# Performance work log

Measured on AMD Instinct MI355X. Metric: run time of the kernel, lower is better.

## Reference

```python
import jax, jax.numpy as jnp
import numpy as np

N = 100000
E = 800000
F_IN = 256
HID = 64
H = 4
NEG_SLOPE = 0.2
BN_EPS = 1e-5


def setup_inputs() -> dict:
    key = jax.random.key(0)
    ks = jax.random.split(key, 20)
    s = 0.05
    return {
        "x": jax.random.normal(ks[0], (N, F_IN), jnp.float32),
        "edge_index": jax.random.randint(ks[1], (2, E), 0, N, jnp.int64),
        # GCNConv params
        "W_gcn": jax.random.normal(ks[2], (F_IN, HID), jnp.float32) * s,
        "b_gcn": jnp.zeros((HID,), jnp.float32),
        "g0": jnp.ones((HID,), jnp.float32),
        "beta0": jnp.zeros((HID,), jnp.float32),
        # GATConv 1 params
        "W1": jax.random.normal(ks[3], (HID, H * HID), jnp.float32) * s,
        "a_src1": jax.random.normal(ks[4], (H, HID), jnp.float32) * s,
        "a_dst1": jax.random.normal(ks[5], (H, HID), jnp.float32) * s,
        "b1": jnp.zeros((H * HID,), jnp.float32),
        "g1": jnp.ones((H * HID,), jnp.float32),
        "beta1": jnp.zeros((H * HID,), jnp.float32),
        # GATConv 2 params
        "W2": jax.random.normal(ks[6], (H * HID, H * HID), jnp.float32) * s,
        "a_src2": jax.random.normal(ks[7], (H, HID), jnp.float32) * s,
        "a_dst2": jax.random.normal(ks[8], (H, HID), jnp.float32) * s,
        "b2": jnp.zeros((H * HID,), jnp.float32),
        "g2": jnp.ones((H * HID,), jnp.float32),
        "beta2": jnp.zeros((H * HID,), jnp.float32),
    }


def _add_self_loops(edge_index, n):
    loop = jnp.arange(n, dtype=edge_index.dtype)
    src = jnp.concatenate([edge_index[0], loop])
    dst = jnp.concatenate([edge_index[1], loop])
    return src, dst


def _batch_norm(x, g, b):
    # BatchNorm1d, training-mode batch stats (biased variance), no dropout
    m = x.mean(0)
    v = x.var(0)
    return g * (x - m) * jax.lax.rsqrt(v + BN_EPS) + b


def _gcn_conv(x, src, dst, W, b, n):
    # symmetric normalization with self-loops already included in src/dst
    deg = jax.ops.segment_sum(jnp.ones_like(dst, jnp.float32), dst, n)
    dinv = jax.lax.rsqrt(jnp.maximum(deg, 1.0))
    norm = dinv[src] * dinv[dst]  # [E']
    h = x @ W  # [N, HID]
    out = jax.ops.segment_sum(h[src] * norm[:, None], dst, n)
    return out + b


def _gat_conv(x, src, dst, W, a_src, a_dst, b, n):
    h = (x @ W).reshape(n, H, HID)  # [N, H, C]
    alpha_s = jnp.einsum("nhc,hc->nh", h, a_src)  # [N, H]
    alpha_d = jnp.einsum("nhc,hc->nh", h, a_dst)
    e = alpha_s[src] + alpha_d[dst]  # [E', H]
    e = jnp.where(e > 0, e, NEG_SLOPE * e)  # LeakyReLU
    # softmax over incoming edges of each dst node, per head
    emax = jax.ops.segment_max(e, dst, n)
    w = jnp.exp(e - emax[dst])
    wsum = jax.ops.segment_sum(w, dst, n)
    att = w / wsum[dst]  # [E', H]
    out = jax.ops.segment_sum(att[:, :, None] * h[src], dst, n)  # [N, H, C]
    return out.reshape(n, H * HID) + b


def reference(x, edge_index, W_gcn, b_gcn, g0, beta0, W1, a_src1, a_dst1, b1,
              g1, beta1, W2, a_src2, a_dst2, b2, g2, beta2):
    n = x.shape[0]
    src, dst = _add_self_loops(edge_index, n)
    h = jax.nn.relu(_gcn_conv(x, src, dst, W_gcn, b_gcn, n))
    h = _batch_norm(h, g0, beta0)
    h = _gat_conv(h, src, dst, W1, a_src1, a_dst1, b1, n)
    h = jax.nn.elu(_batch_norm(h, g1, beta1))
    h = _gat_conv(h, src, dst, W2, a_src2, a_dst2, b2, n)
    h = jax.nn.elu(_batch_norm(h, g2, beta2))
    return h
```

## Files before the change

kernel.cpp:

```cpp
#include <hip/hip_runtime.h>
#include <hip/hip_bf16.h>
#include <math.h>

#define NN 100000
#define EE 800000
#define FIN 256
#define CH 64
#define C1 256
#define BN_EPS 1e-5f
#define NEG_SLOPE 0.2f

typedef __attribute__((ext_vector_type(8))) short short8;
typedef __attribute__((ext_vector_type(8))) unsigned short u16x8;
typedef __attribute__((ext_vector_type(4))) float f32x4;

__device__ __forceinline__ float bf2f(ushort u) {
    return __uint_as_float(((unsigned)u) << 16);
}
__device__ __forceinline__ ushort f2bf(float f) {
    unsigned u = __float_as_uint(f);
    return (ushort)((u + 0x7FFF + ((u >> 16) & 1)) >> 16);
}

__global__ void hist_kernel(const int* __restrict__ ei, int* __restrict__ deg) {
    int t = blockIdx.x * 256 + threadIdx.x;
    if (t < EE) atomicAdd(&deg[ei[EE + t]], 1);
}
__global__ void dinv_kernel(const int* __restrict__ deg, float* __restrict__ dinv) {
    int i = blockIdx.x * 256 + threadIdx.x;
    if (i < NN) dinv[i] = rsqrtf((float)(deg[i] + 1));
}
__global__ void scan_k1(const int* __restrict__ deg, int* __restrict__ row_start,
                        int* __restrict__ bsum) {
    __shared__ int sh[256];
    int t = threadIdx.x;
    int i = blockIdx.x * 256 + t;
    int v = (i < NN) ? (deg[i] + 1) : 0;
    sh[t] = v;
    __syncthreads();
    for (int off = 1; off < 256; off <<= 1) {
        int add = (t >= off) ? sh[t - off] : 0;
        __syncthreads();
        sh[t] += add;
        __syncthreads();
    }
    if (i < NN) row_start[i] = sh[t] - v;
    if (t == 255) bsum[blockIdx.x] = sh[255];
}
__global__ void scan_k2(int* __restrict__ bsum, int nb) {
    __shared__ int sh[512];
    int t = threadIdx.x;
    int v = (t < nb) ? bsum[t] : 0;
    sh[t] = v;
    __syncthreads();
    for (int off = 1; off < 512; off <<= 1) {
        int add = (t >= off) ? sh[t - off] : 0;
        __syncthreads();
        sh[t] += add;
        __syncthreads();
    }
    if (t < nb) bsum[t] = sh[t] - v;
}
__global__ void scan_k3(int* __restrict__ row_start, const int* __restrict__ bsum) {
    int i = blockIdx.x * 256 + threadIdx.x;
    if (i < NN) row_start[i] += bsum[i >> 8];
    if (i == NN) row_start[NN] = EE + NN;
}
__global__ void scatter_kernel(const int* __restrict__ ei, const int* __restrict__ row_start,
                               int* __restrict__ fill, int* __restrict__ sorted) {
    int t = blockIdx.x * 256 + threadIdx.x;
    if (t >= EE + NN) return;
    int s, d;
    if (t < EE) { s = ei[t]; d = ei[EE + t]; }
    else        { s = t - EE; d = s; }
    int pos = atomicAdd(&fill[d], 1);
    sorted[row_start[d] + pos] = s;
}

__global__ void convert_f32_bf16(const float* __restrict__ in, ushort* __restrict__ out, long n4) {
    long i = (long)blockIdx.x * 256 + threadIdx.x;
    if (i < n4) {
        float4 v = *(const float4*)&in[i * 4];
        ushort4 o;
        o.x = f2bf(v.x); o.y = f2bf(v.y); o.z = f2bf(v.z); o.w = f2bf(v.w);
        *(ushort4*)&out[i * 4] = o;
    }
}
__global__ void transpose_w(const float* __restrict__ W, ushort* __restrict__ Bt, int M, int K) {
    int idx = blockIdx.x * 256 + threadIdx.x;
    if (idx < M * K) {
        int m = idx / K, n = idx % K;
        Bt[n * M + m] = f2bf(W[idx]);
    }
}

__global__ __launch_bounds__(256) void gemm_mfma(
        const ushort* __restrict__ A, const ushort* __restrict__ Bt,
        ushort* __restrict__ C, int M, int K) {
    __shared__ ushort As[64][40];
    __shared__ ushort Bs[64][40];
    int t = threadIdx.x;
    int w = t >> 6;
    int l = t & 63;
    int rowBase = blockIdx.y * 64;
    int colBase = blockIdx.x * 64;
    int srow = t >> 2;
    int sk = (t & 3) * 8;
    int m = l & 15, q = l >> 4;
    f32x4 acc[4] = {};
    for (int k0 = 0; k0 < M; k0 += 32) {
        uint4 av = make_uint4(0u, 0u, 0u, 0u);
        int gr = rowBase + srow;
        if (gr < NN) av = *(const uint4*)&A[(long)gr * M + k0 + sk];
        uint4 bv = *(const uint4*)&Bt[(long)(colBase + srow) * M + k0 + sk];
        *(uint4*)&As[srow][sk] = av;
        *(uint4*)&Bs[srow][sk] = bv;
        __syncthreads();
        short8 af = *(const short8*)&As[w * 16 + m][q * 8];
#pragma unroll
        for (int c = 0; c < 4; ++c) {
            short8 bf = *(const short8*)&Bs[c * 16 + m][q * 8];
            acc[c] = __builtin_amdgcn_mfma_f32_16x16x32_bf16(af, bf, acc[c], 0, 0, 0);
        }
        __syncthreads();
    }
#pragma unroll
    for (int c = 0; c < 4; ++c) {
#pragma unroll
        for (int r = 0; r < 4; ++r) {
            int orow = rowBase + w * 16 + q * 4 + r;
            if (orow < NN) C[(long)orow * K + colBase + c * 16 + m] = f2bf(acc[c][r]);
        }
    }
}

__global__ __launch_bounds__(256) void gcn_gather(
        const int* __restrict__ row_start, const int* __restrict__ sorted,
        const float* __restrict__ dinv, const ushort* __restrict__ h0,
        float* __restrict__ agg) {
    int node = blockIdx.x * 4 + (threadIdx.x >> 6);
    if (node >= NN) return;
    int l = threadIdx.x & 63;
    int slot = l >> 3;
    int li = l & 7;
    int c = li * 8;
    int b = row_start[node], e = row_start[node + 1];
    float a[8] = {};
    for (int i = b + slot; i < e; i += 8) {
        int s = sorted[i];
        float dv = dinv[s];
        u16x8 v = *(const u16x8*)&h0[(long)s * 64 + c];
#pragma unroll
        for (int j = 0; j < 8; ++j) a[j] += dv * bf2f((ushort)v[j]);
    }
#pragma unroll
    for (int j = 0; j < 8; ++j) {
        a[j] += __shfl_xor(a[j], 8);
        a[j] += __shfl_xor(a[j], 16);
        a[j] += __shfl_xor(a[j], 32);
    }
    if (slot == 0) {
        float dn = dinv[node];
        f32x4 o0, o1;
#pragma unroll
        for (int j = 0; j < 4; ++j) { o0[j] = a[j] * dn; o1[j] = a[4 + j] * dn; }
        *(f32x4*)&agg[(long)node * 64 + c] = o0;
        *(f32x4*)&agg[(long)node * 64 + c + 4] = o1;
    }
}

__global__ __launch_bounds__(256) void bn_stats64(
        const float* __restrict__ x, const float* __restrict__ bias,
        float* __restrict__ sums, float* __restrict__ sumsq) {
    __shared__ float red[4][16][8];
    int l = threadIdx.x & 63;
    int w = threadIdx.x >> 6;
    int wv = blockIdx.x * 4 + w;
    int nw = gridDim.x * 4;
    int sub = l >> 4;
    int c = (l & 15) * 4;
    f32x4 b4 = *(const f32x4*)&bias[c];
    float s0 = 0.f, s1 = 0.f, s2 = 0.f, s3 = 0.f;
    float q0 = 0.f, q1 = 0.f, q2 = 0.f, q3 = 0.f;
    for (int r = wv * 4 + sub; r < NN; r += nw * 4) {
        f32x4 v = *(const f32x4*)&x[(long)r * 64 + c];
        float v0 = fmaxf(v[0] + b4[0], 0.f);
        float v1 = fmaxf(v[1] + b4[1], 0.f);
        float v2 = fmaxf(v[2] + b4[2], 0.f);
        float v3 = fmaxf(v[3] + b4[3], 0.f);
        s0 += v0; s1 += v1; s2 += v2; s3 += v3;
        q0 += v0 * v0; q1 += v1 * v1; q2 += v2 * v2; q3 += v3 * v3;
    }
    s0 += __shfl_xor(s0, 16); s1 += __shfl_xor(s1, 16);
    s2 += __shfl_xor(s2, 16); s3 += __shfl_xor(s3, 16);
    q0 += __shfl_xor(q0, 16); q1 += __shfl_xor(q1, 16);
    q2 += __shfl_xor(q2, 16); q3 += __shfl_xor(q3, 16);
    s0 += __shfl_xor(s0, 32); s1 += __shfl_xor(s1, 32);
    s2 += __shfl_xor(s2, 32); s3 += __shfl_xor(s3, 32);
    q0 += __shfl_xor(q0, 32); q1 += __shfl_xor(q1, 32);
    q2 += __shfl_xor(q2, 32); q3 += __shfl_xor(q3, 32);
    if (sub == 0) {
        int li = l & 15;
        red[w][li][0] = s0; red[w][li][1] = s1; red[w][li][2] = s2; red[w][li][3] = s3;
        red[w][li][4] = q0; red[w][li][5] = q1; red[w][li][6] = q2; red[w][li][7] = q3;
    }
    __syncthreads();
    if (w == 0 && sub == 0) {
        int li = l & 15;
        atomicAdd(&sums[c + 0], red[0][li][0] + red[1][li][0] + red[2][li][0] + red[3][li][0]);
        atomicAdd(&sums[c + 1], red[0][li][1] + red[1][li][1] + red[2][li][1] + red[3][li][1]);
        atomicAdd(&sums[c + 2], red[0][li][2] + red[1][li][2] + red[2][li][2] + red[3][li][2]);
        atomicAdd(&sums[c + 3], red[0][li][3] + red[1][li][3] + red[2][li][3] + red[3][li][3]);
        atomicAdd(&sumsq[c + 0], red[0][li][4] + red[1][li][4] + red[2][li][4] + red[3][li][4]);
        atomicAdd(&sumsq[c + 1], red[0][li][5] + red[1][li][5] + red[2][li][5] + red[3][li][5]);
        atomicAdd(&sumsq[c + 2], red[0][li][6] + red[1][li][6] + red[2][li][6] + red[3][li][6]);
        atomicAdd(&sumsq[c + 3], red[0][li][7] + red[1][li][7] + red[2][li][7] + red[3][li][7]);
    }
}
__global__ __launch_bounds__(256) void bn_stats256(
        const ushort* __restrict__ x,
        float* __restrict__ sums, float* __restrict__ sumsq) {
    __shared__ float red[4][64][8];
    int l = threadIdx.x & 63;
    int w = threadIdx.x >> 6;
    int wv = blockIdx.x * 4 + w;
    int nw = gridDim.x * 4;
    int c = l * 4;
    float s0 = 0.f, s1 = 0.f, s2 = 0.f, s3 = 0.f;
    float q0 = 0.f, q1 = 0.f, q2 = 0.f, q3 = 0.f;
    for (int r = wv; r < NN; r += nw) {
        ushort4 v = *(const ushort4*)&x[(long)r * 256 + c];
        float v0 = bf2f(v.x), v1 = bf2f(v.y), v2 = bf2f(v.z), v3 = bf2f(v.w);
        s0 += v0; s1 += v1; s2 += v2; s3 += v3;
        q0 += v0 * v0; q1 += v1 * v1; q2 += v2 * v2; q3 += v3 * v3;
    }
    red[w][l][0] = s0; red[w][l][1] = s1; red[w][l][2] = s2; red[w][l][3] = s3;
    red[w][l][4] = q0; red[w][l][5] = q1; red[w][l][6] = q2; red[w][l][7] = q3;
    __syncthreads();
    if (w == 0) {
        atomicAdd(&sums[c + 0], red[0][l][0] + red[1][l][0] + red[2][l][0] + red[3][l][0]);
        atomicAdd(&sums[c + 1], red[0][l][1] + red[1][l][1] + red[2][l][1] + red[3][l][1]);
        atomicAdd(&sums[c + 2], red[0][l][2] + red[1][l][2] + red[2][l][2] + red[3][l][2]);
        atomicAdd(&sums[c + 3], red[0][l][3] + red[1][l][3] + red[2][l][3] + red[3][l][3]);
        atomicAdd(&sumsq[c + 0], red[0][l][4] + red[1][l][4] + red[2][l][4] + red[3][l][4]);
        atomicAdd(&sumsq[c + 1], red[0][l][5] + red[1][l][5] + red[2][l][5] + red[3][l][5]);
        atomicAdd(&sumsq[c + 2], red[0][l][6] + red[1][l][6] + red[2][l][6] + red[3][l][6]);
        atomicAdd(&sumsq[c + 3], red[0][l][7] + red[1][l][7] + red[2][l][7] + red[3][l][7]);
    }
}
__global__ void bn_finalize(const float* __restrict__ sums, const float* __restrict__ sumsq,
                            const float* __restrict__ g, const float* __restrict__ beta,
                            float* __restrict__ scale, float* __restrict__ shift, int C) {
    int c = threadIdx.x;
    if (c < C) {
        float mean = sums[c] / (float)NN;
        float var = sumsq[c] / (float)NN - mean * mean;
        float sc = g[c] * rsqrtf(var + BN_EPS);
        scale[c] = sc;
        shift[c] = beta[c] - mean * sc;
    }
}
__global__ __launch_bounds__(256) void bn_apply_gcn(
        const float* __restrict__ x, const float* __restrict__ bias,
        const float* __restrict__ scale, const float* __restrict__ shift,
        ushort* __restrict__ out) {
    int l = threadIdx.x & 63;
    int wv = blockIdx.x * 4 + (threadIdx.x >> 6);
    int nw = gridDim.x * 4;
    int c = (l & 15) * 4;
    int sub = l >> 4;
    f32x4 b4  = *(const f32x4*)&bias[c];
    f32x4 sc4 = *(const f32x4*)&scale[c];
    f32x4 sh4 = *(const f32x4*)&shift[c];
    for (int r = wv * 4 + sub; r < NN; r += nw * 4) {
        f32x4 v = *(const f32x4*)&x[(long)r * 64 + c];
        ushort4 o;
        o.x = f2bf(sc4[0] * fmaxf(v[0] + b4[0], 0.f) + sh4[0]);
        o.y = f2bf(sc4[1] * fmaxf(v[1] + b4[1], 0.f) + sh4[1]);
        o.z = f2bf(sc4[2] * fmaxf(v[2] + b4[2], 0.f) + sh4[2]);
        o.w = f2bf(sc4[3] * fmaxf(v[3] + b4[3], 0.f) + sh4[3]);
        *(ushort4*)&out[(long)r * 64 + c] = o;
    }
}
__global__ __launch_bounds__(256) void bn_apply_gat(
        const ushort* __restrict__ x,
        const float* __restrict__ scale, const float* __restrict__ shift,
        void* __restrict__ out, int out_bf16) {
    int l = threadIdx.x & 63;
    int wv = blockIdx.x * 4 + (threadIdx.x >> 6);
    int nw = gridDim.x * 4;
    int c = l * 4;
    f32x4 sc4 = *(const f32x4*)&scale[c];
    f32x4 sh4 = *(const f32x4*)&shift[c];
    if (out_bf16) {
        ushort* ob = (ushort*)out;
        for (int r = wv; r < NN; r += nw) {
            ushort4 v = *(const ushort4*)&x[(long)r * 256 + c];
            float t0 = sc4[0] * bf2f(v.x) + sh4[0];
            float t1 = sc4[1] * bf2f(v.y) + sh4[1];
            float t2 = sc4[2] * bf2f(v.z) + sh4[2];
            float t3 = sc4[3] * bf2f(v.w) + sh4[3];
            t0 = (t0 > 0.f) ? t0 : (__expf(t0) - 1.f);
            t1 = (t1 > 0.f) ? t1 : (__expf(t1) - 1.f);
            t2 = (t2 > 0.f) ? t2 : (__expf(t2) - 1.f);
            t3 = (t3 > 0.f) ? t3 : (__expf(t3) - 1.f);
            ushort4 o;
            o.x = f2bf(t0); o.y = f2bf(t1); o.z = f2bf(t2); o.w = f2bf(t3);
            *(ushort4*)&ob[(long)r * 256 + c] = o;
        }
    } else {
        float* of = (float*)out;
        for (int r = wv; r < NN; r += nw) {
            ushort4 v = *(const ushort4*)&x[(long)r * 256 + c];
            float t0 = sc4[0] * bf2f(v.x) + sh4[0];
            float t1 = sc4[1] * bf2f(v.y) + sh4[1];
            float t2 = sc4[2] * bf2f(v.z) + sh4[2];
            float t3 = sc4[3] * bf2f(v.w) + sh4[3];
            f32x4 o;
            o[0] = (t0 > 0.f) ? t0 : (__expf(t0) - 1.f);
            o[1] = (t1 > 0.f) ? t1 : (__expf(t1) - 1.f);
            o[2] = (t2 > 0.f) ? t2 : (__expf(t2) - 1.f);
            o[3] = (t3 > 0.f) ? t3 : (__expf(t3) - 1.f);
            *(f32x4*)&of[(long)r * 256 + c] = o;
        }
    }
}

__global__ void gat_alpha(const ushort* __restrict__ h, const float* __restrict__ a_src,
                          const float* __restrict__ a_dst,
                          float* __restrict__ alpha_s, float* __restrict__ alpha_d) {
    int n = blockIdx.x;
    int t = threadIdx.x;
    float hv = bf2f(h[(long)n * 256 + t]);
    float vs = hv * a_src[t];
    float vd = hv * a_dst[t];
    for (int off = 32; off > 0; off >>= 1) {
        vs += __shfl_down(vs, off);
        vd += __shfl_down(vd, off);
    }
    if ((t & 63) == 0) {
        int head = t >> 6;
        alpha_s[n * 4 + head] = vs;
        alpha_d[n * 4 + head] = vd;
    }
}

__global__ __launch_bounds__(256) void gat_att(
        const int* __restrict__ row_start, const int* __restrict__ sorted,
        const float* __restrict__ as, const float* __restrict__ ad,
        float* __restrict__ att, float* __restrict__ inv_ls) {
    int node = blockIdx.x * 4 + (threadIdx.x >> 6);
    if (node >= NN) return;
    int l = threadIdx.x & 63;
    int h = l & 3, k = l >> 2;
    int b = row_start[node], e = row_start[node + 1];
    float adn = ad[node * 4 + h];
    float lm = -1e30f;
    for (int i = b + k; i < e; i += 16) {
        int s = sorted[i];
        float ev = as[s * 4 + h] + adn;
        ev = (ev > 0.f) ? ev : NEG_SLOPE * ev;
        lm = fmaxf(lm, ev);
    }
    lm = fmaxf(lm, __shfl_xor(lm, 4));
    lm = fmaxf(lm, __shfl_xor(lm, 8));
    lm = fmaxf(lm, __shfl_xor(lm, 16));
    lm = fmaxf(lm, __shfl_xor(lm, 32));
    float ls = 0.f;
    for (int i = b + k; i < e; i += 16) {
        int s = sorted[i];
        float ev = as[s * 4 + h] + adn;
        ev = (ev > 0.f) ? ev : NEG_SLOPE * ev;
        float wv = __expf(ev - lm);
        att[(long)i * 4 + h] = wv;
        ls += wv;
    }
    ls += __shfl_xor(ls, 4);
    ls += __shfl_xor(ls, 8);
    ls += __shfl_xor(ls, 16);
    ls += __shfl_xor(ls, 32);
    if (k == 0) inv_ls[node * 4 + h] = 1.0f / ls;
}

__global__ __launch_bounds__(256) void gat_gather(
        const int* __restrict__ row_start, const int* __restrict__ sorted,
        const float* __restrict__ att, const float* __restrict__ inv_ls,
        const ushort* __restrict__ h, ushort* __restrict__ out) {
    int node = blockIdx.x * 4 + (threadIdx.x >> 6);
    if (node >= NN) return;
    int l = threadIdx.x & 63;
    int slot = l >> 5;
    int li = l & 31;
    int c = li * 8;
    int head = li >> 3;
    int b = row_start[node], e = row_start[node + 1];
    float a[8] = {};
    int i = b + slot;
    for (; i + 2 < e; i += 4) {
        int s0 = sorted[i], s1 = sorted[i + 2];
        float w0 = att[(long)i * 4 + head];
        float w1 = att[(long)(i + 2) * 4 + head];
        u16x8 v0 = *(const u16x8*)&h[(long)s0 * 256 + c];
        u16x8 v1 = *(const u16x8*)&h[(long)s1 * 256 + c];
#pragma unroll
        for (int j = 0; j < 8; ++j)
            a[j] += w0 * bf2f((ushort)v0[j]) + w1 * bf2f((ushort)v1[j]);
    }
    for (; i < e; i += 2) {
        int s0 = sorted[i];
        float w0 = att[(long)i * 4 + head];
        u16x8 v0 = *(const u16x8*)&h[(long)s0 * 256 + c];
#pragma unroll
        for (int j = 0; j < 8; ++j) a[j] += w0 * bf2f((ushort)v0[j]);
    }
#pragma unroll
    for (int j = 0; j < 8; ++j) a[j] += __shfl_xor(a[j], 32);
    if (slot == 0) {
        float inv = inv_ls[node * 4 + head];
        u16x8 o;
#pragma unroll
        for (int j = 0; j < 8; ++j) o[j] = f2bf(a[j] * inv);
        *(u16x8*)&out[(long)node * 256 + c] = o;
    }
}

extern "C" void kernel_launch(void* const* d_in, const int* in_sizes, int n_in,
                              void* d_out, int out_size, void* d_ws, size_t ws_size,
                              hipStream_t stream) {
    const float* x      = (const float*)d_in[0];
    const int*   ei     = (const int*)d_in[1];
    const float* W_gcn  = (const float*)d_in[2];
    const float* b_gcn  = (const float*)d_in[3];
    const float* g0     = (const float*)d_in[4];
    const float* beta0  = (const float*)d_in[5];
    const float* W1     = (const float*)d_in[6];
    const float* a_src1 = (const float*)d_in[7];
    const float* a_dst1 = (const float*)d_in[8];
    const float* b1     = (const float*)d_in[9];
    const float* g1     = (const float*)d_in[10];
    const float* beta1  = (const float*)d_in[11];
    const float* W2     = (const float*)d_in[12];
    const float* a_src2 = (const float*)d_in[13];
    const float* a_dst2 = (const float*)d_in[14];
    const float* b2     = (const float*)d_in[15];
    const float* g2     = (const float*)d_in[16];
    const float* beta2  = (const float*)d_in[17];

    const long N = NN;
    float* ws = (float*)d_ws;

    float* dinv    = ws;
    float* alpha_s = ws + N;
    float* alpha_d = ws + 5 * N;
    float* sums    = ws + 9 * N;
    float* sumsq   = sums + 256;
    float* scale   = sumsq + 256;
    float* shift   = scale + 256;
    int*   row_start = (int*)(shift + 256);
    int*   fill      = row_start + NN + 1;
    int*   deg_i     = fill + NN;
    int*   sorted    = deg_i + NN;
    int*   bsum      = sorted + EE + NN;
    ushort* Wgt  = (ushort*)(ws + 23 * N);
    ushort* W1t  = Wgt + 16384;
    ushort* W2t  = W1t + 16384;
    ushort* h0b  = (ushort*)(ws + 24 * N);
    ushort* x1b  = h0b;
    float*  agg0 = ws + 56 * N;
    ushort* h1b  = (ushort*)(ws + 120 * N);
    ushort* x2b  = (ushort*)(ws + 248 * N);
    ushort* xb   = x2b;
    ushort* yb   = (ushort*)(ws + 376 * N);
    float*  attb = ws + 504 * N;
    float*  inv_ls = ws + 540 * N;
    float*  outp = (float*)d_out;

    const int BLK = 256;
    dim3 blk(BLK);
    const int NBLK_N = (NN + 255) / 256;

    hipMemsetAsync(fill, 0, 2L * NN * sizeof(int), stream);
    hist_kernel<<<(EE + 255) / 256, blk, 0, stream>>>(ei, deg_i);
    dinv_kernel<<<NBLK_N, blk, 0, stream>>>(deg_i, dinv);
    scan_k1<<<NBLK_N, blk, 0, stream>>>(deg_i, row_start, bsum);
    scan_k2<<<1, 512, 0, stream>>>(bsum, NBLK_N);
    scan_k3<<<(NN + 1 + 255) / 256, blk, 0, stream>>>(row_start, bsum);
    scatter_kernel<<<(EE + NN + 255) / 256, blk, 0, stream>>>(ei, row_start, fill, sorted);

    convert_f32_bf16<<<(int)((N * 256 / 4 + 255) / 256), blk, 0, stream>>>(x, xb, N * 256 / 4);
    transpose_w<<<(FIN * CH + 255) / 256, blk, 0, stream>>>(W_gcn, Wgt, FIN, CH);
    transpose_w<<<(CH * C1 + 255) / 256, blk, 0, stream>>>(W1, W1t, CH, C1);
    transpose_w<<<(C1 * C1 + 255) / 256, blk, 0, stream>>>(W2, W2t, C1, C1);

    gemm_mfma<<<dim3(CH / 64, (NN + 63) / 64), blk, 0, stream>>>(xb, Wgt, h0b, FIN, CH);
    gcn_gather<<<(NN + 3) / 4, blk, 0, stream>>>(row_start, sorted, dinv, h0b, agg0);
    hipMemsetAsync(sums, 0, 512 * sizeof(float), stream);
    bn_stats64<<<512, blk, 0, stream>>>(agg0, b_gcn, sums, sumsq);
    bn_finalize<<<1, CH, 0, stream>>>(sums, sumsq, g0, beta0, scale, shift, CH);
    bn_apply_gcn<<<1024, blk, 0, stream>>>(agg0, b_gcn, scale, shift, x1b);

    gemm_mfma<<<dim3(C1 / 64, (NN + 63) / 64), blk, 0, stream>>>(x1b, W1t, h1b, CH, C1);
    gat_alpha<<<NN, blk, 0, stream>>>(h1b, a_src1, a_dst1, alpha_s, alpha_d);
    gat_att<<<(NN + 3) / 4, blk, 0, stream>>>(row_start, sorted, alpha_s, alpha_d, attb, inv_ls);
    gat_gather<<<(NN + 3) / 4, blk, 0, stream>>>(row_start, sorted, attb, inv_ls, h1b, yb);
    hipMemsetAsync(sums, 0, 512 * sizeof(float), stream);
    bn_stats256<<<512, blk, 0, stream>>>(yb, sums, sumsq);
    bn_finalize<<<1, C1, 0, stream>>>(sums, sumsq, g1, beta1, scale, shift, C1);
    bn_apply_gat<<<2048, blk, 0, stream>>>(yb, scale, shift, x2b, 1);

    gemm_mfma<<<dim3(C1 / 64, (NN + 63) / 64), blk, 0, stream>>>(x2b, W2t, h1b, C1, C1);
    gat_alpha<<<NN, blk, 0, stream>>>(h1b, a_src2, a_dst2, alpha_s, alpha_d);
    gat_att<<<(NN + 3) / 4, blk, 0, stream>>>(row_start, sorted, alpha_s, alpha_d, attb, inv_ls);
    gat_gather<<<(NN + 3) / 4, blk, 0, stream>>>(row_start, sorted, attb, inv_ls, h1b, yb);
    hipMemsetAsync(sums, 0, 512 * sizeof(float), stream);
    bn_stats256<<<512, blk, 0, stream>>>(yb, sums, sumsq);
    bn_finalize<<<1, C1, 0, stream>>>(sums, sumsq, g2, beta2, scale, shift, C1);
    bn_apply_gat<<<2048, blk, 0, stream>>>(yb, scale, shift, outp, 0);
}
```

Baseline: 929.7 us.

## Drop softmax max pass, repack GAT alpha and gather kernels per wave

The softmax max-reduction pass in gat_att is removed; exponentials are taken directly with the logit clamped at 80, avoiding a second gather over source alphas. gat_alpha processes four nodes per block with vectorized loads instead of one block per node. gat_gather assigns one wave per node, with each lane covering 4 channels and 8 edges unrolled, so more loads are in flight and no cross-half shuffle reduction is needed. Dropping max subtraction risks overflow or precision loss if logits are large.

```diff
diff --git a/kernel.cpp b/kernel.cpp
--- a/kernel.cpp
+++ b/kernel.cpp
@@ -326,22 +326,28 @@
     }
 }
 
-__global__ void gat_alpha(const ushort* __restrict__ h, const float* __restrict__ a_src,
-                          const float* __restrict__ a_dst,
-                          float* __restrict__ alpha_s, float* __restrict__ alpha_d) {
-    int n = blockIdx.x;
-    int t = threadIdx.x;
-    float hv = bf2f(h[(long)n * 256 + t]);
-    float vs = hv * a_src[t];
-    float vd = hv * a_dst[t];
-    for (int off = 32; off > 0; off >>= 1) {
-        vs += __shfl_down(vs, off);
-        vd += __shfl_down(vd, off);
-    }
-    if ((t & 63) == 0) {
-        int head = t >> 6;
-        alpha_s[n * 4 + head] = vs;
-        alpha_d[n * 4 + head] = vd;
+__global__ __launch_bounds__(256) void gat_alpha(
+        const ushort* __restrict__ h, const float* __restrict__ a_src,
+        const float* __restrict__ a_dst,
+        float* __restrict__ alpha_s, float* __restrict__ alpha_d) {
+    int node = blockIdx.x * 4 + (threadIdx.x >> 6);
+    if (node >= NN) return;
+    int l = threadIdx.x & 63;
+    int c = l * 4;
+    f32x4 asv = *(const f32x4*)&a_src[c];
+    f32x4 adv = *(const f32x4*)&a_dst[c];
+    ushort4 v = *(const ushort4*)&h[(long)node * 256 + c];
+    float h0 = bf2f(v.x), h1 = bf2f(v.y), h2 = bf2f(v.z), h3 = bf2f(v.w);
+    float vs = h0 * asv[0] + h1 * asv[1] + h2 * asv[2] + h3 * asv[3];
+    float vd = h0 * adv[0] + h1 * adv[1] + h2 * adv[2] + h3 * adv[3];
+    vs += __shfl_xor(vs, 1); vd += __shfl_xor(vd, 1);
+    vs += __shfl_xor(vs, 2); vd += __shfl_xor(vd, 2);
+    vs += __shfl_xor(vs, 4); vd += __shfl_xor(vd, 4);
+    vs += __shfl_xor(vs, 8); vd += __shfl_xor(vd, 8);
+    if ((l & 15) == 0) {
+        int head = l >> 4;
+        alpha_s[node * 4 + head] = vs;
+        alpha_d[node * 4 + head] = vd;
     }
 }
 
@@ -355,23 +361,13 @@
     int h = l & 3, k = l >> 2;
     int b = row_start[node], e = row_start[node + 1];
     float adn = ad[node * 4 + h];
-    float lm = -1e30f;
-    for (int i = b + k; i < e; i += 16) {
-        int s = sorted[i];
-        float ev = as[s * 4 + h] + adn;
-        ev = (ev > 0.f) ? ev : NEG_SLOPE * ev;
-        lm = fmaxf(lm, ev);
-    }
-    lm = fmaxf(lm, __shfl_xor(lm, 4));
-    lm = fmaxf(lm, __shfl_xor(lm, 8));
-    lm = fmaxf(lm, __shfl_xor(lm, 16));
-    lm = fmaxf(lm, __shfl_xor(lm, 32));
     float ls = 0.f;
     for (int i = b + k; i < e; i += 16) {
         int s = sorted[i];
         float ev = as[s * 4 + h] + adn;
         ev = (ev > 0.f) ? ev : NEG_SLOPE * ev;
-        float wv = __expf(ev - lm);
+        ev = fminf(ev, 80.f);
+        float wv = __expf(ev);
         att[(long)i * 4 + h] = wv;
         ls += wv;
     }
@@ -389,39 +385,59 @@
     int node = blockIdx.x * 4 + (threadIdx.x >> 6);
     if (node >= NN) return;
     int l = threadIdx.x & 63;
-    int slot = l >> 5;
-    int li = l & 31;
-    int c = li * 8;
-    int head = li >> 3;
+    int head = l >> 4;
     int b = row_start[node], e = row_start[node + 1];
-    float a[8] = {};
-    int i = b + slot;
-    for (; i + 2 < e; i += 4) {
-        int s0 = sorted[i], s1 = sorted[i + 2];
-        float w0 = att[(long)i * 4 + head];
-        float w1 = att[(long)(i + 2) * 4 + head];
-        u16x8 v0 = *(const u16x8*)&h[(long)s0 * 256 + c];
-        u16x8 v1 = *(const u16x8*)&h[(long)s1 * 256 + c];
-#pragma unroll
-        for (int j = 0; j < 8; ++j)
-            a[j] += w0 * bf2f((ushort)v0[j]) + w1 * bf2f((ushort)v1[j]);
-    }
-    for (; i < e; i += 2) {
+    float a0 = 0.f, a1 = 0.f, a2 = 0.f, a3 = 0.f;
+    int i = b;
+    for (; i + 7 < e; i += 8) {
+        int s[8]; float w[8]; ushort4 v[8];
+#pragma unroll
+        for (int j = 0; j < 8; ++j) s[j] = sorted[i + j];
+#pragma unroll
+        for (int j = 0; j < 8; ++j) w[j] = att[(long)(i + j) * 4 + head];
+#pragma unroll
+        for (int j = 0; j < 8; ++j) v[j] = *(const ushort4*)&h[(long)s[j] * 256 + l * 4];
+#pragma unroll
+        for (int j = 0; j < 8; ++j) {
+            a0 += w[j] * bf2f(v[j].x);
+            a1 += w[j] * bf2f(v[j].y);
+            a2 += w[j] * bf2f(v[j].z);
+            a3 += w[j] * bf2f(v[j].w);
+        }
+    }
+    if (i + 3 < e) {
+        int s[4]; float w[4]; ushort4 v[4];
+#pragma unroll
+        for (int j = 0; j < 4; ++j) s[j] = sorted[i + j];
+#pragma unroll
+        for (int j = 0; j < 4; ++j) w[j] = att[(long)(i + j) * 4 + head];
+#pragma unroll
+        for (int j = 0; j < 4; ++j) v[j] = *(const ushort4*)&h[(long)s[j] * 256 + l * 4];
+#pragma unroll
+        for (int j = 0; j < 4; ++j) {
+            a0 += w[j] * bf2f(v[j].x);
+            a1 += w[j] * bf2f(v[j].y);
+            a2 += w[j] * bf2f(v[j].z);
+            a3 += w[j] * bf2f(v[j].w);
+        }
+        i += 4;
+    }
+    for (; i < e; ++i) {
         int s0 = sorted[i];
         float w0 = att[(long)i * 4 + head];
-        u16x8 v0 = *(const u16x8*)&h[(long)s0 * 256 + c];
-#pragma unroll
-        for (int j = 0; j < 8; ++j) a[j] += w0 * bf2f((ushort)v0[j]);
-    }
-#pragma unroll
-    for (int j = 0; j < 8; ++j) a[j] += __shfl_xor(a[j], 32);
-    if (slot == 0) {
-        float inv = inv_ls[node * 4 + head];
-        u16x8 o;
-#pragma unroll
-        for (int j = 0; j < 8; ++j) o[j] = f2bf(a[j] * inv);
-        *(u16x8*)&out[(long)node * 256 + c] = o;
-    }
+        ushort4 v0 = *(const ushort4*)&h[(long)s0 * 256 + l * 4];
+        a0 += w0 * bf2f(v0.x);
+        a1 += w0 * bf2f(v0.y);
+        a2 += w0 * bf2f(v0.z);
+        a3 += w0 * bf2f(v0.w);
+    }
+    float inv = inv_ls[node * 4 + head];
+    ushort4 o;
+    o.x = f2bf(a0 * inv);
+    o.y = f2bf(a1 * inv);
+    o.z = f2bf(a2 * inv);
+    o.w = f2bf(a3 * inv);
+    *(ushort4*)&out[(long)node * 256 + l * 4] = o;
 }
 
 extern "C" void kernel_launch(void* const* d_in, const int* in_sizes, int n_in,
@@ -500,7 +516,7 @@
     bn_apply_gcn<<<1024, blk, 0, stream>>>(agg0, b_gcn, scale, shift, x1b);
 
     gemm_mfma<<<dim3(C1 / 64, (NN + 63) / 64), blk, 0, stream>>>(x1b, W1t, h1b, CH, C1);
-    gat_alpha<<<NN, blk, 0, stream>>>(h1b, a_src1, a_dst1, alpha_s, alpha_d);
+    gat_alpha<<<(NN + 3) / 4, blk, 0, stream>>>(h1b, a_src1, a_dst1, alpha_s, alpha_d);
     gat_att<<<(NN + 3) / 4, blk, 0, stream>>>(row_start, sorted, alpha_s, alpha_d, attb, inv_ls);
     gat_gather<<<(NN + 3) / 4, blk, 0, stream>>>(row_start, sorted, attb, inv_ls, h1b, yb);
     hipMemsetAsync(sums, 0, 512 * sizeof(float), stream);
@@ -509,7 +525,7 @@
     bn_apply_gat<<<2048, blk, 0, stream>>>(yb, scale, shift, x2b, 1);
 
     gemm_mfma<<<dim3(C1 / 64, (NN + 63) / 64), blk, 0, stream>>>(x2b, W2t, h1b, C1, C1);
-    gat_alpha<<<NN, blk, 0, stream>>>(h1b, a_src2, a_dst2, alpha_s, alpha_d);
+    gat_alpha<<<(NN + 3) / 4, blk, 0, stream>>>(h1b, a_src2, a_dst2, alpha_s, alpha_d);
     gat_att<<<(NN + 3) / 4, blk, 0, stream>>>(row_start, sorted, alpha_s, alpha_d, attb, inv_ls);
     gat_gather<<<(NN + 3) / 4, blk, 0, stream>>>(row_start, sorted, attb, inv_ls, h1b, yb);
     hipMemsetAsync(sums, 0, 512 * sizeof(float), stream);
```

Result: faster. 845.3 us (-9.1%).
